# Kernel tuning notes

Measured on AMD Instinct MI355X. Metric: run time of the kernel, lower is better.

The kernel has to match this reference:

```python
import jax, jax.numpy as jnp
import numpy as np
import math

H = 128
HEADS = 2
NEG = -float(1 << 32)
BN_EPS = 1e-5
LN_EPS = 1e-5


def _bn_eval(x, g, b):
    # BatchNorm1d in eval mode with running_mean=0, running_var=1
    return g * (x / jnp.sqrt(1.0 + BN_EPS)) + b


def _ln(x, g, b):
    mu = x.mean(-1, keepdims=True)
    var = ((x - mu) ** 2).mean(-1, keepdims=True)
    return g * (x - mu) / jnp.sqrt(var + LN_EPS) + b


def _multi_embed(tables, idx):
    # tables [F,V,H], idx [N,F] -> sum_f tables[f, idx[:,f]]  (ogb Atom/BondEncoder)
    F = tables.shape[0]
    return tables[jnp.arange(F)[None, :], idx].sum(axis=1)


def _gin_graph(x, edge_attr, edge_index, batch, num_graphs, atom_emb, bond_emb, eps, w1, b1, g1, be1, w2, b2, g2, be2):
    h = _multi_embed(atom_emb, x)  # [N,H]
    tgt, src = edge_index[0], edge_index[1]
    L = eps.shape[0]
    for l in range(L):
        e = _multi_embed(bond_emb[l], edge_attr)  # [E,H]
        msg = jax.nn.relu(h[src] + e)
        agg = jax.ops.segment_sum(msg, tgt, num_segments=h.shape[0])
        z = (1.0 + eps[l]) * h + agg
        z = jax.nn.relu(_bn_eval(z @ w1[l] + b1[l], g1[l], be1[l])) @ w2[l] + b2[l]
        h = _bn_eval(z, g2[l], be2[l])
        if l != L - 1:
            h = jax.nn.relu(h)  # dropout is identity in eval mode
    s = jax.ops.segment_sum(h, batch, num_segments=num_graphs)
    c = jax.ops.segment_sum(jnp.ones_like(h), batch, num_segments=num_graphs)
    return s / (c + 1e-9)  # mean pooling per graph


def _sab(X, wq, bq, wk, bk, wv, bv, wo, bo, l1g, l1b, l2g, l2b):
    # MAB(X, X) with HEADS heads, use_ln=True. X: [B,S,H]
    B, S, _ = X.shape
    dh = H // HEADS

    def split(T):  # torch split(last)+cat(dim0): head-major [HEADS*B, S, dh]
        return T.reshape(B, S, HEADS, dh).transpose(2, 0, 1, 3).reshape(HEADS * B, S, dh)

    Qs, Ks, Vs = split(X @ wq + bq), split(X @ wk + bk), split(X @ wv + bv)
    A = jax.nn.softmax(jnp.einsum('bqd,bkd->bqk', Qs, Ks) / math.sqrt(dh), axis=-1)
    O = Qs + jnp.einsum('bqk,bkd->bqd', A, Vs)
    O = O.reshape(HEADS, B, S, dh).transpose(1, 2, 0, 3).reshape(B, S, H)
    O = _ln(O, l1g, l1b)
    O = _ln(O @ wo + bo, l2g, l2b)
    return O


def setup_inputs() -> dict:
    key = jax.random.key(0)
    ks = iter(jax.random.split(key, 64))
    nk = lambda: next(ks)
    V, L = 64, 4
    NS, ES = 60000, 140000
    NM, EM = 150000, 350000
    S, M, D, B = 492, 600, 200, 64
    f32 = jnp.float32
    w = lambda *shp: jax.random.normal(nk(), shp, f32) * 0.05
    inp = {}
    inp['atom_emb'] = w(2, 9, V, H)
    inp['bond_emb'] = w(2, L, 3, V, H)
    inp['gin_eps'] = jnp.zeros((2, L), f32)
    inp['gin_w1'] = w(2, L, H, 2 * H); inp['gin_b1'] = jnp.zeros((2, L, 2 * H), f32)
    inp['gin_bn1_g'] = jnp.ones((2, L, 2 * H), f32); inp['gin_bn1_b'] = jnp.zeros((2, L, 2 * H), f32)
    inp['gin_w2'] = w(2, L, 2 * H, H); inp['gin_b2'] = jnp.zeros((2, L, H), f32)
    inp['gin_bn2_g'] = jnp.ones((2, L, H), f32); inp['gin_bn2_b'] = jnp.zeros((2, L, H), f32)
    for nm in ['sab_wq', 'sab_wk', 'sab_wv', 'sab_wo']:
        inp[nm] = w(H, H)
    for nm in ['sab_bq', 'sab_bk', 'sab_bv', 'sab_bo', 'sab_ln1_b', 'sab_ln2_b']:
        inp[nm] = jnp.zeros((H,), f32)
    inp['sab_ln1_g'] = jnp.ones((H,), f32); inp['sab_ln2_g'] = jnp.ones((H,), f32)
    inp['agg_wq'] = w(H, H); inp['agg_bq'] = jnp.zeros((H,), f32)
    inp['agg_wk'] = w(H, H); inp['agg_bk'] = jnp.zeros((H,), f32)
    inp['score_w1'] = w(H, H // 2); inp['score_b1'] = jnp.zeros((H // 2,), f32)
    inp['score_w2'] = w(H // 2, 1); inp['score_b2'] = jnp.zeros((1,), f32)
    inp['patient_emb'] = jax.random.uniform(nk(), (B, S), f32)
    inp['average_projection'] = jax.random.uniform(nk(), (D, M), f32) / M
    inp['sub_x'] = jax.random.randint(nk(), (NS, 9), 0, V)
    inp['sub_edge_attr'] = jax.random.randint(nk(), (ES, 3), 0, V)
    inp['sub_edge_index'] = jax.random.randint(nk(), (2, ES), 0, NS)
    inp['sub_batch'] = jax.random.randint(nk(), (NS,), 0, S)
    inp['mol_x'] = jax.random.randint(nk(), (NM, 9), 0, V)
    inp['mol_edge_attr'] = jax.random.randint(nk(), (EM, 3), 0, V)
    inp['mol_edge_index'] = jax.random.randint(nk(), (2, EM), 0, NM)
    inp['mol_batch'] = jax.random.randint(nk(), (NM,), 0, M)
    mask = jax.random.bernoulli(nk(), 0.3, (D, S))
    inp['mask'] = mask.at[:, 0].set(False)
    inp['num_sub'] = S
    inp['num_mol'] = M
    return inp


def reference(atom_emb, bond_emb, gin_eps, gin_w1, gin_b1, gin_bn1_g, gin_bn1_b, gin_w2, gin_b2, gin_bn2_g, gin_bn2_b, sab_wq, sab_bq, sab_wk, sab_bk, sab_wv, sab_bv, sab_wo, sab_bo, sab_ln1_g, sab_ln1_b, sab_ln2_g, sab_ln2_b, agg_wq, agg_bq, agg_wk, agg_bk, score_w1, score_b1, score_w2, score_b2, patient_emb, average_projection, sub_x, sub_edge_attr, sub_edge_index, sub_batch, mol_x, mol_edge_attr, mol_edge_index, mol_batch, mask, num_sub, num_mol):
    # substructure encoder (GINGraph #0) + SAB interaction
    sub = _gin_graph(sub_x, sub_edge_attr, sub_edge_index, sub_batch, num_sub, atom_emb[0], bond_emb[0], gin_eps[0], gin_w1[0], gin_b1[0], gin_bn1_g[0], gin_bn1_b[0], gin_w2[0], gin_b2[0], gin_bn2_g[0], gin_bn2_b[0])
    sub = _sab(sub[None], sab_wq, sab_bq, sab_wk, sab_bk, sab_wv, sab_bv, sab_wo, sab_bo, sab_ln1_g, sab_ln1_b, sab_ln2_g, sab_ln2_b)[0]  # [S,H]
    # molecule encoder (GINGraph #1) + drug-level averaging
    mol = _gin_graph(mol_x, mol_edge_attr, mol_edge_index, mol_batch, num_mol, atom_emb[1], bond_emb[1], gin_eps[1], gin_w1[1], gin_b1[1], gin_bn1_g[1], gin_bn1_b[1], gin_w2[1], gin_b2[1], gin_bn2_g[1], gin_bn2_b[1])
    mol_emb = average_projection @ mol  # [D,H]
    # AttnAgg: masked attention, per-patient reweighting via diag(fix_feat)
    Q = mol_emb @ agg_wq + agg_bq
    K = sub @ agg_wk + agg_bk
    attn = (Q @ K.T) / math.sqrt(H)
    attn = jax.nn.softmax(jnp.where(mask, NEG, attn), axis=-1)  # [D,S]
    agg = jnp.einsum('ds,bs,sh->bdh', attn, patient_emb, sub)  # [B,D,H]
    logits = (jax.nn.relu(agg @ score_w1 + score_b1) @ score_w2 + score_b2)[..., 0]
    return jax.nn.sigmoid(logits)  # y_prob [B,D]
```

## Files before the change

### kernel.cpp

```cpp
#include <hip/hip_runtime.h>


typedef short short8 __attribute__((ext_vector_type(8)));
typedef unsigned short us8 __attribute__((ext_vector_type(8)));
typedef float f32x4 __attribute__((ext_vector_type(4)));
typedef unsigned short us4 __attribute__((ext_vector_type(4)));
typedef unsigned int u32;

#define BN_RSQ 0.9999950000374997f
#define LN_EPS 1e-5f
#define NEGBIG -4294967296.0f

__device__ __forceinline__ unsigned short f2bf(float x) {
  union { float f; unsigned int u; } v; v.f = x;
  unsigned int r = v.u + 0x7fffu + ((v.u >> 16) & 1u);
  return (unsigned short)(r >> 16);
}
__device__ __forceinline__ float bf2f(unsigned short x) {
  union { unsigned int u; float f; } v; v.u = ((unsigned int)x) << 16;
  return v.f;
}

__global__ __launch_bounds__(256) void prep_all(
    const float* __restrict__ w1, const float* __restrict__ w2,
    unsigned short* __restrict__ w1t, unsigned short* __restrict__ w2t,
    const float* __restrict__ bond, unsigned short* __restrict__ bt16, int bonde,
    const unsigned char* __restrict__ m, int* __restrict__ flags, int maskn) {
  __shared__ int lf[2];
  int b = blockIdx.x;
  if (b < 1024) {
    int i = b * 256 + threadIdx.x;
    int gl = i >> 15;
    int k1 = (i >> 8) & 127, c1 = i & 255;
    w1t[(gl << 15) + c1 * 128 + k1] = f2bf(w1[i]);
    int k2 = (i >> 7) & 255, c2 = i & 127;
    w2t[(gl << 15) + c2 * 256 + k2] = f2bf(w2[i]);
    return;
  }
  if (b < 1792) {
    int i = (b - 1024) * 256 + threadIdx.x;
    if (i < bonde) bt16[i] = f2bf(bond[i]);
    return;
  }
  if (threadIdx.x == 0) { lf[0] = 0; lf[1] = 0; }
  __syncthreads();
  int f0 = 0, f1 = 0;
  for (int i = (b - 1792) * 256 + threadIdx.x; i < maskn; i += 64 * 256) {
    if (m[i]) { if ((i & 3) == 0) f0 = 1; else f1 = 1; }
  }
  if (f0) atomicOr(&lf[0], 1);
  if (f1) atomicOr(&lf[1], 1);
  __syncthreads();
  if (threadIdx.x == 0) {
    if (lf[0]) atomicOr(flags, 1);
    if (lf[1]) atomicOr(flags + 1, 1);
  }
}

__global__ void build_count(const int* __restrict__ ei_m, int Em,
                            const int* __restrict__ ei_s, int Es,
                            const int* __restrict__ bm, int Nm,
                            const int* __restrict__ bs, int Ns,
                            int* __restrict__ deg_e, int* __restrict__ deg_n,
                            int M, int NmR) {
  int i = blockIdx.x * 256 + threadIdx.x;
  if (i < Em) { atomicAdd(&deg_e[ei_m[i]], 1); return; }
  i -= Em;
  if (i < Es) { atomicAdd(&deg_e[NmR + ei_s[i]], 1); return; }
  i -= Es;
  if (i < Nm) { atomicAdd(&deg_n[bm[i]], 1); return; }
  i -= Nm;
  if (i < Ns) { atomicAdd(&deg_n[M + bs[i]], 1); }
}

__global__ __launch_bounds__(256) void scan_block2(
    const int* __restrict__ cntE, int nE, int* __restrict__ exclE, int* __restrict__ bsumE, int nbE,
    const int* __restrict__ cntN, int nN, int* __restrict__ exclN, int* __restrict__ bsumN) {
  const int* cnt; int n; int* excl; int* bsum; int blk;
  if (blockIdx.x < (unsigned)nbE) { cnt = cntE; n = nE; excl = exclE; bsum = bsumE; blk = blockIdx.x; }
  else { cnt = cntN; n = nN; excl = exclN; bsum = bsumN; blk = blockIdx.x - nbE; }
  int gid = blk * 256 + threadIdx.x;
  int lane = threadIdx.x & 63, w = threadIdx.x >> 6;
  int v = (gid < n) ? cnt[gid] : 0;
  int x = v;
#pragma unroll
  for (int off = 1; off < 64; off <<= 1) {
    int y = __shfl_up(x, off, 64);
    if (lane >= off) x += y;
  }
  __shared__ int wt[4];
  if (lane == 63) wt[w] = x;
  __syncthreads();
  int add = 0;
  for (int i = 0; i < w; i++) add += wt[i];
  x += add;
  if (gid < n) excl[gid] = x - v;
  if (threadIdx.x == 255) bsum[blk] = x;
}

__global__ __launch_bounds__(1024) void scan_top2(int* __restrict__ bsumE, int nE,
                                                  int* __restrict__ bsumN, int nN) {
  int* bsum = blockIdx.x ? bsumN : bsumE;
  int n = blockIdx.x ? nN : nE;
  int t = threadIdx.x;
  int lane = t & 63, w = t >> 6;
  int v = (t < n) ? bsum[t] : 0;
  int x = v;
#pragma unroll
  for (int off = 1; off < 64; off <<= 1) {
    int y = __shfl_up(x, off, 64);
    if (lane >= off) x += y;
  }
  __shared__ int wt[16];
  if (lane == 63) wt[w] = x;
  __syncthreads();
  int add = 0;
  for (int i = 0; i < w; i++) add += wt[i];
  x += add;
  if (t < n) bsum[t] = x - v;
}

__global__ void finalize2(const int* __restrict__ exclE, const int* __restrict__ bsumE,
                          int nE, int totE, int* __restrict__ rowE,
                          const int* __restrict__ exclN, const int* __restrict__ bsumN,
                          int nN, int totN, int* __restrict__ rowN) {
  int i = blockIdx.x * 256 + threadIdx.x;
  if (i <= nE) {
    rowE[i] = (i < nE) ? (exclE[i] + bsumE[i >> 8]) : totE;
    return;
  }
  int j = i - nE - 1;
  if (j <= nN) rowN[j] = (j < nN) ? (exclN[j] + bsumN[j >> 8]) : totN;
}

__global__ void scatter2(const int* __restrict__ ei_m, const int* __restrict__ ea_m, int Em,
                         const int* __restrict__ ei_s, const int* __restrict__ ea_s, int Es, int NmR,
                         const int* __restrict__ rowptr_e, int* __restrict__ cur_e,
                         int2* __restrict__ epool,
                         const int* __restrict__ bm, int Nm,
                         const int* __restrict__ bs, int Ns, int M,
                         const int* __restrict__ rowptr_n, int* __restrict__ cur_n,
                         int* __restrict__ npool) {
  int i = blockIdx.x * 256 + threadIdx.x;
  if (i < Em + Es) {
    int g, src, a0, a1, a2;
    if (i < Em) {
      g = ei_m[i]; src = ei_m[Em + i];
      a0 = ea_m[i * 3]; a1 = ea_m[i * 3 + 1]; a2 = ea_m[i * 3 + 2];
    } else {
      int j = i - Em;
      g = NmR + ei_s[j]; src = NmR + ei_s[Es + j];
      a0 = ea_s[j * 3]; a1 = ea_s[j * 3 + 1]; a2 = ea_s[j * 3 + 2];
    }
    int slot = rowptr_e[g] + atomicAdd(&cur_e[g], 1);
    epool[slot] = make_int2(src * 128, a0 | (a1 << 6) | (a2 << 12));
    return;
  }
  int k = i - (Em + Es);
  if (k >= Nm + Ns) return;
  int g, node;
  if (k < Nm) { g = bm[k]; node = k; }
  else { int j = k - Nm; g = M + bs[j]; node = NmR + j; }
  int slot = rowptr_n[g] + atomicAdd(&cur_n[g], 1);
  npool[slot] = node;
}

__global__ void embed2(const int* __restrict__ xm, const int* __restrict__ xs,
                       const float* __restrict__ atab, int Nm, int Ns, int NmR,
                       unsigned short* __restrict__ h) {
  int i = blockIdx.x * 256 + threadIdx.x;
  const int* x; const float* table; int n, cq, outn;
  if (i < Nm * 32) {
    n = i >> 5; cq = (i & 31) * 4; x = xm; table = atab + (size_t)9 * 64 * 128; outn = n;
  } else {
    int j = i - Nm * 32;
    if (j >= Ns * 32) return;
    n = j >> 5; cq = (j & 31) * 4; x = xs; table = atab; outn = NmR + n;
  }
  float4 s = make_float4(0.f, 0.f, 0.f, 0.f);
#pragma unroll
  for (int f = 0; f < 9; f++) {
    int v = x[n * 9 + f];
    float4 tv = *(const float4*)(table + (size_t)(f * 64 + v) * 128 + cq);
    s.x += tv.x; s.y += tv.y; s.z += tv.z; s.w += tv.w;
  }
  us4 o;
  o.x = f2bf(s.x); o.y = f2bf(s.y); o.z = f2bf(s.z); o.w = f2bf(s.w);
  *(us4*)(h + (size_t)outn * 128 + cq) = o;
}

__global__ __launch_bounds__(256, 4) void gin_fused3(
    const unsigned short* __restrict__ hin, unsigned short* __restrict__ hout,
    const float* __restrict__ eps_all, int l, int NmR,
    const unsigned short* __restrict__ bt16,
    const int2* __restrict__ epool, const int* __restrict__ rowptr_e,
    const unsigned short* __restrict__ w1t_a, const float* __restrict__ b1_a,
    const float* __restrict__ g1_a, const float* __restrict__ be1_a,
    const unsigned short* __restrict__ w2t_a, const float* __restrict__ b2_a,
    const float* __restrict__ g2_a, const float* __restrict__ be2_a) {
  __shared__ __align__(16) unsigned char smem[38144];
  unsigned short* z1s = (unsigned short*)smem;
  unsigned short* zs  = (unsigned short*)(smem + 20736);
  int2* recs = (int2*)smem;
  const int CAP = 2592;
  int t = threadIdx.x;
  int r0 = blockIdx.x * 64;
  int g = (r0 < NmR) ? 1 : 0;
  int gl = g * 4 + l;
  const unsigned short* bt = bt16 + (size_t)gl * 3 * 64 * 128;
  const unsigned short* w1t = w1t_a + (size_t)gl * 32768;
  const unsigned short* w2t = w2t_a + (size_t)gl * 32768;
  const float* b1 = b1_a + gl * 256;
  const float* g1 = g1_a + gl * 256;
  const float* be1 = be1_a + gl * 256;
  const float* b2 = b2_a + gl * 128;
  const float* g2 = g2_a + gl * 128;
  const float* be2 = be2_a + gl * 128;
  float eps1 = 1.0f + eps_all[gl];
  int do_relu = (l != 3);

  int e0 = rowptr_e[r0], e1 = rowptr_e[r0 + 64];
  int nE = e1 - e0;
  int nstage = (nE < CAP) ? nE : CAP;
  for (int i = t; i < nstage; i += 256) recs[i] = epool[e0 + i];
  __syncthreads();

#pragma unroll
  for (int p = 0; p < 2; p++) {
    int lr = p * 32 + (t >> 3);
    int n = r0 + lr;
    int cb = (t & 7) * 16;
    float lo[8], hi[8];
    {
      const u32* hr = (const u32*)(hin + (size_t)n * 128 + cb);
      uint4 h0v = *(const uint4*)hr;
      uint4 h1v = *(const uint4*)(hr + 4);
      u32 hd[8] = {h0v.x, h0v.y, h0v.z, h0v.w, h1v.x, h1v.y, h1v.z, h1v.w};
#pragma unroll
      for (int j = 0; j < 8; j++) {
        lo[j] = eps1 * __uint_as_float(hd[j] << 16);
        hi[j] = eps1 * __uint_as_float(hd[j] & 0xffff0000u);
      }
    }
    int le0 = rowptr_e[n] - e0, le1 = rowptr_e[n + 1] - e0;
    for (int li = le0; li < le1; li++) {
      int2 rec = (li < CAP) ? recs[li] : epool[e0 + li];
      u32 ab = (u32)rec.y;
      const u32* hs = (const u32*)(hin + rec.x + cb);
      const u32* q0 = (const u32*)(bt + (ab & 63u) * 128 + cb);
      const u32* q1 = (const u32*)(bt + (64 + ((ab >> 6) & 63u)) * 128 + cb);
      const u32* q2 = (const u32*)(bt + (128 + ((ab >> 12) & 63u)) * 128 + cb);
      uint4 A0 = *(const uint4*)hs, A1 = *(const uint4*)(hs + 4);
      uint4 B0 = *(const uint4*)q0, B1 = *(const uint4*)(q0 + 4);
      uint4 C0 = *(const uint4*)q1, C1 = *(const uint4*)(q1 + 4);
      uint4 D0 = *(const uint4*)q2, D1 = *(const uint4*)(q2 + 4);
      u32 ad[8] = {A0.x, A0.y, A0.z, A0.w, A1.x, A1.y, A1.z, A1.w};
      u32 bd[8] = {B0.x, B0.y, B0.z, B0.w, B1.x, B1.y, B1.z, B1.w};
      u32 cd[8] = {C0.x, C0.y, C0.z, C0.w, C1.x, C1.y, C1.z, C1.w};
      u32 dd[8] = {D0.x, D0.y, D0.z, D0.w, D1.x, D1.y, D1.z, D1.w};
#pragma unroll
      for (int j = 0; j < 8; j++) {
        float sl = __uint_as_float(ad[j] << 16) + __uint_as_float(bd[j] << 16)
                 + __uint_as_float(cd[j] << 16) + __uint_as_float(dd[j] << 16);
        float sh = __uint_as_float(ad[j] & 0xffff0000u) + __uint_as_float(bd[j] & 0xffff0000u)
                 + __uint_as_float(cd[j] & 0xffff0000u) + __uint_as_float(dd[j] & 0xffff0000u);
        lo[j] += fmaxf(sl, 0.f);
        hi[j] += fmaxf(sh, 0.f);
      }
    }
    u32 od[8];
#pragma unroll
    for (int j = 0; j < 8; j++)
      od[j] = (u32)f2bf(lo[j]) | (((u32)f2bf(hi[j])) << 16);
    u32* zr = (u32*)(zs + lr * 136 + cb);
    *(uint4*)zr = make_uint4(od[0], od[1], od[2], od[3]);
    *(uint4*)(zr + 4) = make_uint4(od[4], od[5], od[6], od[7]);
  }
  __syncthreads();

  int lane = t & 63, wave = t >> 6;
  int quad = lane >> 4, l16 = lane & 15;
  {
    short8 bw[4][4];
    int cb = wave * 64;
#pragma unroll
    for (int nt = 0; nt < 4; nt++) {
      const unsigned short* p = w1t + (cb + nt * 16 + l16) * 128 + quad * 8;
#pragma unroll
      for (int kc = 0; kc < 4; kc++) bw[nt][kc] = *(const short8*)(p + kc * 32);
    }
    for (int mt = 0; mt < 4; mt++) {
      short8 af[4];
      const unsigned short* zrow = zs + (mt * 16 + l16) * 136 + quad * 8;
#pragma unroll
      for (int kc = 0; kc < 4; kc++)
        af[kc] = *(const short8*)(zrow + kc * 32);
#pragma unroll
      for (int nt = 0; nt < 4; nt++) {
        f32x4 acc = {0.f, 0.f, 0.f, 0.f};
#pragma unroll
        for (int kc = 0; kc < 4; kc++)
          acc = __builtin_amdgcn_mfma_f32_16x16x32_bf16(af[kc], bw[nt][kc], acc, 0, 0, 0);
        int c = cb + nt * 16 + l16;
        float sc = g1[c] * BN_RSQ, sh = be1[c], bb = b1[c];
#pragma unroll
        for (int reg = 0; reg < 4; reg++) {
          int r = mt * 16 + quad * 4 + reg;
          float y = (acc[reg] + bb) * sc + sh;
          z1s[r * 264 + c] = f2bf(fmaxf(y, 0.f));
        }
      }
      __syncthreads();
    }
  }
  {
    short8 bw[2][8];
    int cb = wave * 32;
#pragma unroll
    for (int nt = 0; nt < 2; nt++) {
      const unsigned short* p = w2t + (cb + nt * 16 + l16) * 256 + quad * 8;
#pragma unroll
      for (int kc = 0; kc < 8; kc++) bw[nt][kc] = *(const short8*)(p + kc * 32);
    }
    for (int mt = 0; mt < 4; mt++) {
      short8 af[8];
      const unsigned short* zrow = z1s + (mt * 16 + l16) * 264 + quad * 8;
#pragma unroll
      for (int kc = 0; kc < 8; kc++)
        af[kc] = *(const short8*)(zrow + kc * 32);
      __syncthreads();
#pragma unroll
      for (int nt = 0; nt < 2; nt++) {
        f32x4 acc = {0.f, 0.f, 0.f, 0.f};
#pragma unroll
        for (int kc = 0; kc < 8; kc++)
          acc = __builtin_amdgcn_mfma_f32_16x16x32_bf16(af[kc], bw[nt][kc], acc, 0, 0, 0);
        int c = cb + nt * 16 + l16;
        float sc = g2[c] * BN_RSQ, sh = be2[c], bb = b2[c];
#pragma unroll
        for (int reg = 0; reg < 4; reg++) {
          int r = mt * 16 + quad * 4 + reg;
          float y = (acc[reg] + bb) * sc + sh;
          if (do_relu) y = fmaxf(y, 0.f);
          z1s[r * 264 + c] = f2bf(y);
        }
      }
    }
  }
  __syncthreads();
  for (int i = t; i < 1024; i += 256) {
    int r = i >> 4, c8 = (i & 15) * 8;
    us8 v = *(const us8*)(z1s + r * 264 + c8);
    *(us8*)(hout + (size_t)(r0 + r) * 128 + c8) = v;
  }
}

__global__ __launch_bounds__(128) void pool_csr(const unsigned short* __restrict__ h,
                                                const int* __restrict__ npool,
                                                const int* __restrict__ rowptr_n,
                                                float* __restrict__ pooled, int nseg) {
  int m = blockIdx.x;
  if (m >= nseg) return;
  int st = rowptr_n[m];
  int e = rowptr_n[m + 1];
  int len = e - st;
  int c = threadIdx.x;
  float s = 0.f;
  int i = st;
  for (; i + 3 < e; i += 4) {
    int n0 = npool[i], n1 = npool[i + 1], n2 = npool[i + 2], n3 = npool[i + 3];
    float v0 = bf2f(h[(size_t)n0 * 128 + c]);
    float v1 = bf2f(h[(size_t)n1 * 128 + c]);
    float v2 = bf2f(h[(size_t)n2 * 128 + c]);
    float v3 = bf2f(h[(size_t)n3 * 128 + c]);
    s += (v0 + v1) + (v2 + v3);
  }
  for (; i < e; i++) s += bf2f(h[(size_t)npool[i] * 128 + c]);
  pooled[m * 128 + c] = s / ((float)len + 1e-9f);
}

__global__ __launch_bounds__(256) void gemm_tile(const float* __restrict__ A, const float* __restrict__ W,
                                                 const float* __restrict__ bias, float* __restrict__ C,
                                                 int K) {
  __shared__ float As[608];
  __shared__ float red[128];
  int r = blockIdx.x;
  int t = threadIdx.x;
  for (int i = t; i < K; i += 256) As[i] = A[(size_t)r * K + i];
  __syncthreads();
  int c = t & 127, half = t >> 7;
  int Kh = K >> 1;
  int k0 = half * Kh, k1 = k0 + Kh;
  float acc = 0.f;
#pragma unroll 8
  for (int k = k0; k < k1; k++) acc = fmaf(As[k], W[(size_t)k * 128 + c], acc);
  if (half) red[c] = acc;
  __syncthreads();
  if (!half) {
    float v = acc + red[c] + (bias ? bias[c] : 0.f);
    C[(size_t)r * 128 + c] = v;
  }
}

__global__ __launch_bounds__(256) void gemm_qkv(const float* __restrict__ A,
                                                const float* __restrict__ W0, const float* __restrict__ bi0, float* __restrict__ C0,
                                                const float* __restrict__ W1, const float* __restrict__ bi1, float* __restrict__ C1,
                                                const float* __restrict__ W2, const float* __restrict__ bi2, float* __restrict__ C2) {
  __shared__ float As[128];
  __shared__ float red[128];
  int r = blockIdx.x, which = blockIdx.y;
  const float* W = (which == 0) ? W0 : (which == 1) ? W1 : W2;
  const float* bias = (which == 0) ? bi0 : (which == 1) ? bi1 : bi2;
  float* C = (which == 0) ? C0 : (which == 1) ? C1 : C2;
  int t = threadIdx.x;
  if (t < 128) As[t] = A[(size_t)r * 128 + t];
  __syncthreads();
  int c = t & 127, half = t >> 7;
  int k0 = half * 64, k1 = k0 + 64;
  float acc = 0.f;
#pragma unroll 8
  for (int k = k0; k < k1; k++) acc = fmaf(As[k], W[(size_t)k * 128 + c], acc);
  if (half) red[c] = acc;
  __syncthreads();
  if (!half) C[(size_t)r * 128 + c] = acc + red[c] + bias[c];
}

__global__ __launch_bounds__(256) void gemm_aggqk(
    const float* __restrict__ Aq, const float* __restrict__ Wq, const float* __restrict__ bq,
    float* __restrict__ Cq, int D,
    const float* __restrict__ Ak, const float* __restrict__ Wk, const float* __restrict__ bk,
    float* __restrict__ Ck) {
  __shared__ float As[128];
  __shared__ float red[128];
  int r = blockIdx.x;
  const float* A; const float* W; const float* bias; float* C; int rr;
  if (r < D) { A = Aq; W = Wq; bias = bq; C = Cq; rr = r; }
  else { A = Ak; W = Wk; bias = bk; C = Ck; rr = r - D; }
  int t = threadIdx.x;
  if (t < 128) As[t] = A[(size_t)rr * 128 + t];
  __syncthreads();
  int c = t & 127, half = t >> 7;
  int k0 = half * 64, k1 = k0 + 64;
  float acc = 0.f;
#pragma unroll 8
  for (int k = k0; k < k1; k++) acc = fmaf(As[k], W[(size_t)k * 128 + c], acc);
  if (half) red[c] = acc;
  __syncthreads();
  if (!half) C[(size_t)rr * 128 + c] = acc + red[c] + bias[c];
}

__global__ __launch_bounds__(256) void gemm_wo_ln(const float* __restrict__ A,
                                                  const float* __restrict__ W, const float* __restrict__ bias,
                                                  const float* __restrict__ lg, const float* __restrict__ lb,
                                                  float* __restrict__ subf) {
  __shared__ float As[128];
  __shared__ float row[128];
  __shared__ float red2[4];
  int r = blockIdx.x;
  int t = threadIdx.x;
  if (t < 128) As[t] = A[(size_t)r * 128 + t];
  __syncthreads();
  int c = t & 127, half = t >> 7;
  int k0 = half * 64, k1 = k0 + 64;
  float acc = 0.f;
#pragma unroll 8
  for (int k = k0; k < k1; k++) acc = fmaf(As[k], W[(size_t)k * 128 + c], acc);
  if (half) row[c] = acc;
  __syncthreads();
  if (!half) row[c] = acc + row[c] + bias[c];
  __syncthreads();
  if (t < 128) {
    float x = row[t];
    float s = x;
    for (int off = 32; off; off >>= 1) s += __shfl_down(s, off);
    if ((t & 63) == 0) red2[t >> 6] = s;
  }
  __syncthreads();
  if (t < 128) {
    float mu = (red2[0] + red2[1]) * (1.f / 128.f);
    float dd = row[t] - mu;
    float v = dd * dd;
    for (int off = 32; off; off >>= 1) v += __shfl_down(v, off);
    if ((t & 63) == 0) red2[2 + (t >> 6)] = v;
  }
  __syncthreads();
  if (t < 128) {
    float mu = (red2[0] + red2[1]) * (1.f / 128.f);
    float var = (red2[2] + red2[3]) * (1.f / 128.f);
    float dd = row[t] - mu;
    subf[(size_t)r * 128 + t] = lg[t] * dd * rsqrtf(var + LN_EPS) + lb[t];
  }
}

__global__ __launch_bounds__(256) void sab_attn(const float* __restrict__ Q, const float* __restrict__ K,
                                                const float* __restrict__ V, float* __restrict__ O, int S) {
  int q = blockIdx.x, hd = blockIdx.y;
  int t = threadIdx.x;
  __shared__ float sc[512];
  __shared__ float red[8];
  __shared__ float pacc[4][64];
  const float* qrow = Q + q * 128 + hd * 64;
  for (int k = t; k < 512; k += 256) {
    float d = -1e30f;
    if (k < S) {
      const float* krow = K + k * 128 + hd * 64;
      d = 0.f;
#pragma unroll
      for (int j = 0; j < 64; j += 4) {
        float4 a = *(const float4*)(qrow + j);
        float4 b = *(const float4*)(krow + j);
        d += a.x * b.x + a.y * b.y + a.z * b.z + a.w * b.w;
      }
      d *= 0.125f;
    }
    sc[k] = d;
  }
  __syncthreads();
  float m = fmaxf(sc[t], sc[t + 256]);
  for (int off = 32; off; off >>= 1) m = fmaxf(m, __shfl_down(m, off));
  if ((t & 63) == 0) red[t >> 6] = m;
  __syncthreads();
  m = fmaxf(fmaxf(red[0], red[1]), fmaxf(red[2], red[3]));
  float p0 = __expf(sc[t] - m), p1 = __expf(sc[t + 256] - m);
  sc[t] = p0; sc[t + 256] = p1;
  float s = p0 + p1;
  for (int off = 32; off; off >>= 1) s += __shfl_down(s, off);
  if ((t & 63) == 0) red[4 + (t >> 6)] = s;
  __syncthreads();
  float inv = 1.f / (red[4] + red[5] + red[6] + red[7]);
  int d = t & 63, part = t >> 6;
  float acc = 0.f;
  for (int k = part; k < S; k += 4) acc += sc[k] * V[k * 128 + hd * 64 + d];
  pacc[part][d] = acc;
  __syncthreads();
  if (part == 0) {
    float o = (pacc[0][d] + pacc[1][d] + pacc[2][d] + pacc[3][d]) * inv;
    O[q * 128 + hd * 64 + d] = qrow[d] + o;
  }
}

__global__ __launch_bounds__(128) void ln_rows(const float* __restrict__ in, float* __restrict__ out,
                                               const float* __restrict__ g, const float* __restrict__ b) {
  int r = blockIdx.x, t = threadIdx.x;
  __shared__ float red[4];
  float x = in[r * 128 + t];
  float s = x;
  for (int off = 32; off; off >>= 1) s += __shfl_down(s, off);
  if ((t & 63) == 0) red[t >> 6] = s;
  __syncthreads();
  float mu = (red[0] + red[1]) * (1.f / 128.f);
  float dd = x - mu;
  float v = dd * dd;
  for (int off = 32; off; off >>= 1) v += __shfl_down(v, off);
  if ((t & 63) == 0) red[2 + (t >> 6)] = v;
  __syncthreads();
  float var = (red[2] + red[3]) * (1.f / 128.f);
  out[r * 128 + t] = g[t] * dd * rsqrtf(var + LN_EPS) + b[t];
}

__global__ __launch_bounds__(256) void agg_attn(const float* __restrict__ Q, const float* __restrict__ Kt,
                                                const void* __restrict__ mask, const int* __restrict__ flags,
                                                float* __restrict__ attn, int D, int S) {
  int d = blockIdx.x, t = threadIdx.x;
  __shared__ float sc[512];
  __shared__ float red[8];
  int layout = (flags[1] == 0) ? 0 : (flags[0] ? 1 : 2);
  const float* qrow = Q + d * 128;
  for (int s = t; s < 512; s += 256) {
    float v = NEGBIG;
    if (s < S) {
      int mi = d * S + s;
      bool msk;
      if (layout == 0)      msk = ((const int*)mask)[mi] != 0;
      else if (layout == 1) msk = ((const unsigned char*)mask)[mi] != 0;
      else                  msk = ((const float*)mask)[mi] != 0.f;
      if (!msk) {
        float dd = 0.f;
        const float* krow = Kt + s * 128;
#pragma unroll
        for (int j = 0; j < 128; j += 4) {
          float4 a = *(const float4*)(qrow + j);
          float4 b = *(const float4*)(krow + j);
          dd += a.x * b.x + a.y * b.y + a.z * b.z + a.w * b.w;
        }
        v = dd * 0.08838834764831845f;
      }
    }
    sc[s] = v;
  }
  __syncthreads();
  float m = fmaxf(sc[t], sc[t + 256]);
  for (int off = 32; off; off >>= 1) m = fmaxf(m, __shfl_down(m, off));
  if ((t & 63) == 0) red[t >> 6] = m;
  __syncthreads();
  m = fmaxf(fmaxf(red[0], red[1]), fmaxf(red[2], red[3]));
  float p0 = __expf(sc[t] - m), p1 = __expf(sc[t + 256] - m);
  float s2 = p0 + p1;
  for (int off = 32; off; off >>= 1) s2 += __shfl_down(s2, off);
  if ((t & 63) == 0) red[4 + (t >> 6)] = s2;
  __syncthreads();
  float inv = 1.f / (red[4] + red[5] + red[6] + red[7]);
  attn[d * S + t] = p0 * inv;
  if (t + 256 < S) attn[d * S + t + 256] = p1 * inv;
}

__global__ void prep_subT(const float* __restrict__ subf, unsigned short* __restrict__ subT, int S) {
  int i = blockIdx.x * 256 + threadIdx.x;
  if (i >= 128 * 512) return;
  int hh = i >> 9, k = i & 511;
  subT[i] = (k < S) ? f2bf(subf[k * 128 + hh]) : (unsigned short)0;
}

__global__ __launch_bounds__(256) void agg_mfma(const float* __restrict__ attn, const float* __restrict__ pat,
                                                const unsigned short* __restrict__ subT,
                                                float* __restrict__ aggT, int D, int S) {
  int d = blockIdx.x, t = threadIdx.x;
  __shared__ unsigned short As[64][40];
  int lane = t & 63, wave = t >> 6;
  int quad = lane >> 4, l16 = lane & 15;
  f32x4 acc[8];
#pragma unroll
  for (int nt = 0; nt < 8; nt++) acc[nt] = (f32x4){0.f, 0.f, 0.f, 0.f};
  const float* arow = attn + d * S;
  int srow = t >> 2, skb = (t & 3) * 8;
  for (int c = 0; c < 16; c++) {
    int s0 = c * 32;
    __syncthreads();
    unsigned short v[8];
#pragma unroll
    for (int j = 0; j < 8; j++) {
      int s = s0 + skb + j;
      float x = (s < S) ? arow[s] * pat[srow * S + s] : 0.f;
      v[j] = f2bf(x);
    }
    *(us4*)&As[srow][skb]     = *(us4*)&v[0];
    *(us4*)&As[srow][skb + 4] = *(us4*)&v[4];
    __syncthreads();
    short8 af = *(const short8*)&As[16 * wave + l16][quad * 8];
#pragma unroll
    for (int nt = 0; nt < 8; nt++) {
      short8 bf = *(const short8*)(subT + (nt * 16 + l16) * 512 + s0 + quad * 8);
      acc[nt] = __builtin_amdgcn_mfma_f32_16x16x32_bf16(af, bf, acc[nt], 0, 0, 0);
    }
  }
#pragma unroll
  for (int nt = 0; nt < 8; nt++) {
    int hh = nt * 16 + l16;
#pragma unroll
    for (int reg = 0; reg < 4; reg++) {
      int b = 16 * wave + quad * 4 + reg;
      aggT[((size_t)(b * D + d)) * 128 + hh] = acc[nt][reg];
    }
  }
}

__global__ __launch_bounds__(256) void score_head(const float* __restrict__ aggT,
                                                  const float* __restrict__ w1, const float* __restrict__ b1,
                                                  const float* __restrict__ w2, const float* __restrict__ b2,
                                                  float* __restrict__ out, int total) {
  int i = blockIdx.x * 4 + (threadIdx.x >> 6);
  int j = threadIdx.x & 63;
  if (i >= total) return;
  const float* av = aggT + (size_t)i * 128;
  float acc = b1[j];
#pragma unroll 8
  for (int k = 0; k < 128; k++) acc = fmaf(av[k], w1[k * 64 + j], acc);
  acc = fmaxf(acc, 0.f) * w2[j];
  for (int off = 32; off; off >>= 1) acc += __shfl_down(acc, off);
  if (j == 0) {
    float x = acc + b2[0];
    out[i] = 1.f / (1.f + __expf(-x));
  }
}

extern "C" void kernel_launch(void* const* d_in, const int* in_sizes, int n_in,
                              void* d_out, int out_size, void* d_ws, size_t ws_size,
                              hipStream_t stream) {
  const float* atom_emb = (const float*)d_in[0];
  const float* bond_emb = (const float*)d_in[1];
  const float* gin_eps  = (const float*)d_in[2];
  const float* gin_w1   = (const float*)d_in[3];
  const float* gin_b1   = (const float*)d_in[4];
  const float* bn1g     = (const float*)d_in[5];
  const float* bn1b     = (const float*)d_in[6];
  const float* gin_w2   = (const float*)d_in[7];
  const float* gin_b2   = (const float*)d_in[8];
  const float* bn2g     = (const float*)d_in[9];
  const float* bn2b     = (const float*)d_in[10];
  const float* sab_wq = (const float*)d_in[11];
  const float* sab_wk = (const float*)d_in[12];
  const float* sab_wv = (const float*)d_in[13];
  const float* sab_wo = (const float*)d_in[14];
  const float* sab_bq = (const float*)d_in[15];
  const float* sab_bk = (const float*)d_in[16];
  const float* sab_bv = (const float*)d_in[17];
  const float* sab_bo = (const float*)d_in[18];
  const float* ln1b = (const float*)d_in[19];
  const float* ln2b = (const float*)d_in[20];
  const float* ln1g = (const float*)d_in[21];
  const float* ln2g = (const float*)d_in[22];
  const float* agg_wq = (const float*)d_in[23];
  const float* agg_bq = (const float*)d_in[24];
  const float* agg_wk = (const float*)d_in[25];
  const float* agg_bk = (const float*)d_in[26];
  const float* score_w1 = (const float*)d_in[27];
  const float* score_b1 = (const float*)d_in[28];
  const float* score_w2 = (const float*)d_in[29];
  const float* score_b2 = (const float*)d_in[30];
  const float* patient  = (const float*)d_in[31];
  const float* avgproj  = (const float*)d_in[32];
  const int* sub_x     = (const int*)d_in[33];
  const int* sub_ea    = (const int*)d_in[34];
  const int* sub_ei    = (const int*)d_in[35];
  const int* sub_batch = (const int*)d_in[36];
  const int* mol_x     = (const int*)d_in[37];
  const int* mol_ea    = (const int*)d_in[38];
  const int* mol_ei    = (const int*)d_in[39];
  const int* mol_batch = (const int*)d_in[40];
  const void* mask     = d_in[41];

  const int Ns = in_sizes[33] / 9, Es = in_sizes[34] / 3;
  const int Nm = in_sizes[37] / 9, Em = in_sizes[38] / 3;
  const int S = 492, M = 600, D = 200, B = 64;
  const int NmR = (Nm + 63) & ~63;
  const int NsR = (Ns + 63) & ~63;
  const int NTOT = NmR + NsR;
  const int NSEG = M + S;
  const int ETOT = Em + Es;
  const int BONDE = 2 * 4 * 3 * 64 * 128;

  char* Wp = (char*)d_ws;
  size_t off = 0;
  auto alloc = [&](size_t bytes) -> void* {
    void* p = Wp + off;
    off = (off + bytes + 255) & ~(size_t)255;
    return p;
  };
  unsigned short* h0 = (unsigned short*)alloc((size_t)NTOT * 128 * 2);
  unsigned short* h1 = (unsigned short*)alloc((size_t)NTOT * 128 * 2);
  unsigned short* w1t = (unsigned short*)alloc(262144 * 2);
  unsigned short* w2t = (unsigned short*)alloc(262144 * 2);
  unsigned short* bt16 = (unsigned short*)alloc((size_t)BONDE * 2);
  int2* epool  = (int2*)alloc((size_t)ETOT * 8);
  int*  npool  = (int*)alloc((size_t)(Nm + Ns) * 4);
  int*  excl_e = (int*)alloc((size_t)NTOT * 4);
  int*  bsum_e = (int*)alloc(1024 * 4);
  int*  excl_n = (int*)alloc((size_t)NSEG * 4);
  int*  bsum_n = (int*)alloc(1024 * 4);
  int*  rowptr_e = (int*)alloc((size_t)(NTOT + 1) * 4);
  int*  rowptr_n = (int*)alloc((size_t)(NSEG + 1) * 4);
  char* zstart = Wp + off;
  int*  deg_e  = (int*)alloc((size_t)NTOT * 4);
  int*  deg_n  = (int*)alloc((size_t)NSEG * 4);
  int*  cur_e  = (int*)alloc((size_t)NTOT * 4);
  int*  cur_n  = (int*)alloc((size_t)NSEG * 4);
  int*  flags  = (int*)alloc(8);
  size_t zsize = (size_t)((Wp + off) - zstart);
  float* pooled_all = (float*)alloc((size_t)NSEG * 128 * 4);
  float* pooled_mol = pooled_all;
  float* pooled_sub = pooled_all + (size_t)M * 128;
  float* Qb   = (float*)alloc((size_t)S * 128 * 4);
  float* Kb   = (float*)alloc((size_t)S * 128 * 4);
  float* Vb   = (float*)alloc((size_t)S * 128 * 4);
  float* Ob   = (float*)alloc((size_t)S * 128 * 4);
  float* subf = (float*)alloc((size_t)S * 128 * 4);
  unsigned short* subT = (unsigned short*)alloc((size_t)128 * 512 * 2);
  float* mol_embb = (float*)alloc((size_t)D * 128 * 4);
  float* aggQb = (float*)alloc((size_t)D * 128 * 4);
  float* aggKb = (float*)alloc((size_t)S * 128 * 4);
  float* attnb = (float*)alloc((size_t)D * S * 4);
  float* aggTb = (float*)alloc((size_t)B * D * 128 * 4);
  (void)ws_size; (void)n_in; (void)out_size;

  hipMemsetAsync(zstart, 0, zsize, stream);
  prep_all<<<1856, 256, 0, stream>>>(gin_w1, gin_w2, w1t, w2t,
                                     bond_emb, bt16, BONDE,
                                     (const unsigned char*)mask, flags, D * S);

  int total_cnt = Em + Es + Nm + Ns;
  build_count<<<(total_cnt + 255) / 256, 256, 0, stream>>>(
      mol_ei, Em, sub_ei, Es, mol_batch, Nm, sub_batch, Ns, deg_e, deg_n, M, NmR);
  int nb_e = (NTOT + 255) / 256;
  int nb_n = (NSEG + 255) / 256;
  scan_block2<<<nb_e + nb_n, 256, 0, stream>>>(deg_e, NTOT, excl_e, bsum_e, nb_e,
                                               deg_n, NSEG, excl_n, bsum_n);
  scan_top2<<<2, 1024, 0, stream>>>(bsum_e, nb_e, bsum_n, nb_n);
  finalize2<<<((NTOT + 1) + (NSEG + 1) + 1 + 255) / 256, 256, 0, stream>>>(
      excl_e, bsum_e, NTOT, ETOT, rowptr_e,
      excl_n, bsum_n, NSEG, Nm + Ns, rowptr_n);
  scatter2<<<(ETOT + Nm + Ns + 255) / 256, 256, 0, stream>>>(
      mol_ei, mol_ea, Em, sub_ei, sub_ea, Es, NmR, rowptr_e, cur_e, epool,
      mol_batch, Nm, sub_batch, Ns, M, rowptr_n, cur_n, npool);

  embed2<<<((Nm + Ns) * 32 + 255) / 256, 256, 0, stream>>>(
      mol_x, sub_x, atom_emb, Nm, Ns, NmR, h0);
  unsigned short* hin = h0; unsigned short* hout = h1;
  for (int l = 0; l < 4; l++) {
    gin_fused3<<<NTOT / 64, 256, 0, stream>>>(
        hin, hout, gin_eps, l, NmR, bt16, epool, rowptr_e,
        w1t, gin_b1, bn1g, bn1b, w2t, gin_b2, bn2g, bn2b);
    unsigned short* tmp = hin; hin = hout; hout = tmp;
  }
  pool_csr<<<NSEG, 128, 0, stream>>>(hin, npool, rowptr_n, pooled_all, NSEG);

  gemm_qkv<<<dim3(S, 3), 256, 0, stream>>>(pooled_sub,
                                           sab_wq, sab_bq, Qb,
                                           sab_wk, sab_bk, Kb,
                                           sab_wv, sab_bv, Vb);
  sab_attn<<<dim3(S, 2), 256, 0, stream>>>(Qb, Kb, Vb, Ob, S);
  ln_rows<<<S, 128, 0, stream>>>(Ob, Ob, ln1g, ln1b);
  gemm_wo_ln<<<S, 256, 0, stream>>>(Ob, sab_wo, sab_bo, ln2g, ln2b, subf);
  prep_subT<<<(128 * 512 + 255) / 256, 256, 0, stream>>>(subf, subT, S);

  gemm_tile<<<D, 256, 0, stream>>>(avgproj, pooled_mol, (const float*)nullptr, mol_embb, 600);

  gemm_aggqk<<<D + S, 256, 0, stream>>>(mol_embb, agg_wq, agg_bq, aggQb, D,
                                        subf, agg_wk, agg_bk, aggKb);
  agg_attn<<<D, 256, 0, stream>>>(aggQb, aggKb, mask, flags, attnb, D, S);
  agg_mfma<<<D, 256, 0, stream>>>(attnb, patient, subT, aggTb, D, S);
  score_head<<<(B * D + 3) / 4, 256, 0, stream>>>(aggTb, score_w1, score_b1, score_w2, score_b2,
                                                  (float*)d_out, B * D);
}
```

Baseline: 963.5 us.

## Fuse agg attention with MFMA aggregation, fold subT transpose, split pooling

Merges agg_attn and agg_mfma into one kernel that keeps the softmax row in shared memory, so the attn buffer round trip and one launch go away. gemm_wo_ln now writes the transposed bf16 sub matrix directly, which removes the prep_subT kernel. subT moves into the zero-initialised region so padded columns are still zero. pool_csr uses 256 threads, stages node indices in shared memory and splits each segment between two thread groups to get more parallelism.

```diff
diff --git a/kernel.cpp b/kernel.cpp
--- a/kernel.cpp
+++ b/kernel.cpp
@@ -355,28 +355,40 @@
   }
 }
 
-__global__ __launch_bounds__(128) void pool_csr(const unsigned short* __restrict__ h,
+__global__ __launch_bounds__(256) void pool_csr(const unsigned short* __restrict__ h,
                                                 const int* __restrict__ npool,
                                                 const int* __restrict__ rowptr_n,
                                                 float* __restrict__ pooled, int nseg) {
+  __shared__ int nls[512];
+  __shared__ float part[128];
   int m = blockIdx.x;
   if (m >= nseg) return;
   int st = rowptr_n[m];
-  int e = rowptr_n[m + 1];
-  int len = e - st;
-  int c = threadIdx.x;
+  int len = rowptr_n[m + 1] - st;
+  int c = threadIdx.x & 127, grp = threadIdx.x >> 7;
   float s = 0.f;
-  int i = st;
-  for (; i + 3 < e; i += 4) {
-    int n0 = npool[i], n1 = npool[i + 1], n2 = npool[i + 2], n3 = npool[i + 3];
-    float v0 = bf2f(h[(size_t)n0 * 128 + c]);
-    float v1 = bf2f(h[(size_t)n1 * 128 + c]);
-    float v2 = bf2f(h[(size_t)n2 * 128 + c]);
-    float v3 = bf2f(h[(size_t)n3 * 128 + c]);
-    s += (v0 + v1) + (v2 + v3);
-  }
-  for (; i < e; i++) s += bf2f(h[(size_t)npool[i] * 128 + c]);
-  pooled[m * 128 + c] = s / ((float)len + 1e-9f);
+  for (int base = 0; base < len; base += 512) {
+    int cnt = (len - base < 512) ? (len - base) : 512;
+    __syncthreads();
+    for (int i = threadIdx.x; i < cnt; i += 256) nls[i] = npool[st + base + i];
+    __syncthreads();
+    int hh = (cnt + 1) >> 1;
+    int i0 = grp * hh;
+    int i1 = i0 + hh; if (i1 > cnt) i1 = cnt;
+    int i = i0;
+    for (; i + 3 < i1; i += 4) {
+      int n0 = nls[i], n1 = nls[i + 1], n2 = nls[i + 2], n3 = nls[i + 3];
+      float v0 = bf2f(h[(size_t)n0 * 128 + c]);
+      float v1 = bf2f(h[(size_t)n1 * 128 + c]);
+      float v2 = bf2f(h[(size_t)n2 * 128 + c]);
+      float v3 = bf2f(h[(size_t)n3 * 128 + c]);
+      s += (v0 + v1) + (v2 + v3);
+    }
+    for (; i < i1; i++) s += bf2f(h[(size_t)nls[i] * 128 + c]);
+  }
+  if (grp) part[c] = s;
+  __syncthreads();
+  if (!grp) pooled[(size_t)m * 128 + c] = (s + part[c]) / ((float)len + 1e-9f);
 }
 
 __global__ __launch_bounds__(256) void gemm_tile(const float* __restrict__ A, const float* __restrict__ W,
@@ -452,7 +464,8 @@
 __global__ __launch_bounds__(256) void gemm_wo_ln(const float* __restrict__ A,
                                                   const float* __restrict__ W, const float* __restrict__ bias,
                                                   const float* __restrict__ lg, const float* __restrict__ lb,
-                                                  float* __restrict__ subf) {
+                                                  float* __restrict__ subf,
+                                                  unsigned short* __restrict__ subT) {
   __shared__ float As[128];
   __shared__ float row[128];
   __shared__ float red2[4];
@@ -488,7 +501,9 @@
     float mu = (red2[0] + red2[1]) * (1.f / 128.f);
     float var = (red2[2] + red2[3]) * (1.f / 128.f);
     float dd = row[t] - mu;
-    subf[(size_t)r * 128 + t] = lg[t] * dd * rsqrtf(var + LN_EPS) + lb[t];
+    float val = lg[t] * dd * rsqrtf(var + LN_EPS) + lb[t];
+    subf[(size_t)r * 128 + t] = val;
+    subT[(size_t)t * 512 + r] = f2bf(val);
   }
 }
 
@@ -558,12 +573,15 @@
   out[r * 128 + t] = g[t] * dd * rsqrtf(var + LN_EPS) + b[t];
 }
 
-__global__ __launch_bounds__(256) void agg_attn(const float* __restrict__ Q, const float* __restrict__ Kt,
-                                                const void* __restrict__ mask, const int* __restrict__ flags,
-                                                float* __restrict__ attn, int D, int S) {
+__global__ __launch_bounds__(256) void agg_fused(const float* __restrict__ Q, const float* __restrict__ Kt,
+                                                 const void* __restrict__ mask, const int* __restrict__ flags,
+                                                 const float* __restrict__ pat,
+                                                 const unsigned short* __restrict__ subT,
+                                                 float* __restrict__ aggT, int D, int S) {
   int d = blockIdx.x, t = threadIdx.x;
   __shared__ float sc[512];
   __shared__ float red[8];
+  __shared__ unsigned short As[64][40];
   int layout = (flags[1] == 0) ? 0 : (flags[0] ? 1 : 2);
   const float* qrow = Q + d * 128;
   for (int s = t; s < 512; s += 256) {
@@ -600,28 +618,15 @@
   if ((t & 63) == 0) red[4 + (t >> 6)] = s2;
   __syncthreads();
   float inv = 1.f / (red[4] + red[5] + red[6] + red[7]);
-  attn[d * S + t] = p0 * inv;
-  if (t + 256 < S) attn[d * S + t + 256] = p1 * inv;
-}
-
-__global__ void prep_subT(const float* __restrict__ subf, unsigned short* __restrict__ subT, int S) {
-  int i = blockIdx.x * 256 + threadIdx.x;
-  if (i >= 128 * 512) return;
-  int hh = i >> 9, k = i & 511;
-  subT[i] = (k < S) ? f2bf(subf[k * 128 + hh]) : (unsigned short)0;
-}
-
-__global__ __launch_bounds__(256) void agg_mfma(const float* __restrict__ attn, const float* __restrict__ pat,
-                                                const unsigned short* __restrict__ subT,
-                                                float* __restrict__ aggT, int D, int S) {
-  int d = blockIdx.x, t = threadIdx.x;
-  __shared__ unsigned short As[64][40];
+  sc[t] = p0 * inv;
+  sc[t + 256] = p1 * inv;
+  __syncthreads();
+
   int lane = t & 63, wave = t >> 6;
   int quad = lane >> 4, l16 = lane & 15;
   f32x4 acc[8];
 #pragma unroll
   for (int nt = 0; nt < 8; nt++) acc[nt] = (f32x4){0.f, 0.f, 0.f, 0.f};
-  const float* arow = attn + d * S;
   int srow = t >> 2, skb = (t & 3) * 8;
   for (int c = 0; c < 16; c++) {
     int s0 = c * 32;
@@ -630,7 +635,7 @@
 #pragma unroll
     for (int j = 0; j < 8; j++) {
       int s = s0 + skb + j;
-      float x = (s < S) ? arow[s] * pat[srow * S + s] : 0.f;
+      float x = (s < S) ? sc[s] * pat[srow * S + s] : 0.f;
       v[j] = f2bf(x);
     }
     *(us4*)&As[srow][skb]     = *(us4*)&v[0];
@@ -755,6 +760,7 @@
   int*  cur_e  = (int*)alloc((size_t)NTOT * 4);
   int*  cur_n  = (int*)alloc((size_t)NSEG * 4);
   int*  flags  = (int*)alloc(8);
+  unsigned short* subT = (unsigned short*)alloc((size_t)128 * 512 * 2);
   size_t zsize = (size_t)((Wp + off) - zstart);
   float* pooled_all = (float*)alloc((size_t)NSEG * 128 * 4);
   float* pooled_mol = pooled_all;
@@ -764,11 +770,9 @@
   float* Vb   = (float*)alloc((size_t)S * 128 * 4);
   float* Ob   = (float*)alloc((size_t)S * 128 * 4);
   float* subf = (float*)alloc((size_t)S * 128 * 4);
-  unsigned short* subT = (unsigned short*)alloc((size_t)128 * 512 * 2);
   float* mol_embb = (float*)alloc((size_t)D * 128 * 4);
   float* aggQb = (float*)alloc((size_t)D * 128 * 4);
   float* aggKb = (float*)alloc((size_t)S * 128 * 4);
-  float* attnb = (float*)alloc((size_t)D * S * 4);
   float* aggTb = (float*)alloc((size_t)B * D * 128 * 4);
   (void)ws_size; (void)n_in; (void)out_size;
 
@@ -801,7 +805,7 @@
         w1t, gin_b1, bn1g, bn1b, w2t, gin_b2, bn2g, bn2b);
     unsigned short* tmp = hin; hin = hout; hout = tmp;
   }
-  pool_csr<<<NSEG, 128, 0, stream>>>(hin, npool, rowptr_n, pooled_all, NSEG);
+  pool_csr<<<NSEG, 256, 0, stream>>>(hin, npool, rowptr_n, pooled_all, NSEG);
 
   gemm_qkv<<<dim3(S, 3), 256, 0, stream>>>(pooled_sub,
                                            sab_wq, sab_bq, Qb,
@@ -809,15 +813,13 @@
                                            sab_wv, sab_bv, Vb);
   sab_attn<<<dim3(S, 2), 256, 0, stream>>>(Qb, Kb, Vb, Ob, S);
   ln_rows<<<S, 128, 0, stream>>>(Ob, Ob, ln1g, ln1b);
-  gemm_wo_ln<<<S, 256, 0, stream>>>(Ob, sab_wo, sab_bo, ln2g, ln2b, subf);
-  prep_subT<<<(128 * 512 + 255) / 256, 256, 0, stream>>>(subf, subT, S);
+  gemm_wo_ln<<<S, 256, 0, stream>>>(Ob, sab_wo, sab_bo, ln2g, ln2b, subf, subT);
 
   gemm_tile<<<D, 256, 0, stream>>>(avgproj, pooled_mol, (const float*)nullptr, mol_embb, 600);
 
   gemm_aggqk<<<D + S, 256, 0, stream>>>(mol_embb, agg_wq, agg_bq, aggQb, D,
                                         subf, agg_wk, agg_bk, aggKb);
-  agg_attn<<<D, 256, 0, stream>>>(aggQb, aggKb, mask, flags, attnb, D, S);
-  agg_mfma<<<D, 256, 0, stream>>>(attnb, patient, subT, aggTb, D, S);
+  agg_fused<<<D, 256, 0, stream>>>(aggQb, aggKb, mask, flags, patient, subT, aggTb, D, S);
   score_head<<<(B * D + 3) / 4, 256, 0, stream>>>(aggTb, score_w1, score_b1, score_w2, score_b2,
                                                   (float*)d_out, B * D);
 }
```

After: 945.6 us. No clear change (-1.9%).
